# Optimization experiments

Hardware: AMD Instinct MI355X
Metric: run time of the kernel (lower is better)

Reference implementation:

```python
import jax, jax.numpy as jnp
import numpy as np


def setup_inputs() -> dict:
    key = jax.random.key(0)
    k1, k2, k3 = jax.random.split(key, 3)
    B, C, N, T = 32, 64, 1024, 64
    x = jax.random.normal(k1, (B, C, N, T), dtype=jnp.float32)
    W = jax.random.normal(k2, (T, T), dtype=jnp.float32) * 0.05
    alpha = jax.random.normal(k3, (C,), dtype=jnp.float32) * 0.1
    return {"x": x, "W": W, "alpha": alpha}


def reference(x, W, alpha):
    # x: [B, C, N, T]; channel-weighted reduction -> Q = K: [B, N, T]
    q = jnp.einsum('bcnt,c->bnt', x, alpha)
    # bilinear scores: K @ W @ Q^T -> [B, N, N]
    scores = jnp.einsum('bnt,ts,bms->bnm', q, W, q)
    return jax.nn.softmax(scores, axis=-1)
```

## Files before the change

kernel.cpp:

```cpp
#include <hip/hip_runtime.h>

#define B_ 32
#define C_ 64
#define N_ 1024
#define T_ 64

typedef __attribute__((ext_vector_type(8))) _Float16 half8;
typedef __attribute__((ext_vector_type(4))) _Float16 half4;
typedef __attribute__((ext_vector_type(4))) float f32x4;

__global__ __launch_bounds__(256) void k_q(const float* __restrict__ x,
                                           const float* __restrict__ alpha,
                                           _Float16* __restrict__ q_h) {
    const int bid = blockIdx.x;
    const int s1  = (bid & 7) * 256 + (bid >> 3);
    const int b   = s1 >> 6;
    const int n0  = (s1 & 63) * 16;
    const int tid = threadIdx.x;

    const f32x4* xb = (const f32x4*)(x + (size_t)b * C_ * N_ * T_
                                       + (size_t)n0 * T_);
    f32x4 acc = {0.f, 0.f, 0.f, 0.f};
#pragma unroll 4
    for (int c = 0; c < C_; ++c) {
        f32x4 v = __builtin_nontemporal_load(&xb[(size_t)c * (N_ * T_ / 4) + tid]);
        const float ac = alpha[c];
        acc[0] += ac * v[0]; acc[1] += ac * v[1];
        acc[2] += ac * v[2]; acc[3] += ac * v[3];
    }

    half4 h;
#pragma unroll
    for (int j = 0; j < 4; ++j) h[j] = (_Float16)acc[j];
    *(half4*)(q_h + ((size_t)b * N_ + n0) * T_ + (size_t)tid * 4) = h;
}

__global__ __launch_bounds__(512, 4) void k_scores_softmax(
        const _Float16* __restrict__ q_h,
        const float* __restrict__ W,
        float* __restrict__ out) {
    const int bid = blockIdx.x;
    const int s   = (bid & 7) * 128 + (bid >> 3);
    const int b   = s >> 5;
    const int n0  = (s & 31) * 32;
    const int tid  = threadIdx.x;
    const int w    = tid >> 6;
    const int lane = tid & 63;
    const int lr   = lane & 15;
    const int lk   = lane >> 4;

    __shared__ float Ws[T_][T_];
    __shared__ _Float16 qwh[32][72];
    __shared__ float red[32][8];

    {
        const f32x4* Wv = (const f32x4*)W;
        f32x4* Wd = (f32x4*)&Ws[0][0];
        Wd[tid]       = Wv[tid];
        Wd[tid + 512] = Wv[tid + 512];
    }
    __syncthreads();

    {
        const int tr = w >> 2, tc = w & 3;
        const size_t ar = ((size_t)b * N_ + n0 + tr * 16 + lr) * T_ + lk * 8;
        half8 a0 = *(const half8*)(q_h + ar);
        half8 a1 = *(const half8*)(q_h + ar + 32);
        half8 bh0, bh1, bl0, bl1;
#pragma unroll
        for (int j = 0; j < 8; ++j) {
            const float wv0 = Ws[lk * 8 + j][tc * 16 + lr];
            const float wv1 = Ws[lk * 8 + 32 + j][tc * 16 + lr];
            const _Float16 h0 = (_Float16)wv0;
            const _Float16 h1 = (_Float16)wv1;
            bh0[j] = h0; bl0[j] = (_Float16)(wv0 - (float)h0);
            bh1[j] = h1; bl1[j] = (_Float16)(wv1 - (float)h1);
        }
        f32x4 a = {0.f, 0.f, 0.f, 0.f};
        a = __builtin_amdgcn_mfma_f32_16x16x32_f16(a0, bh0, a, 0, 0, 0);
        a = __builtin_amdgcn_mfma_f32_16x16x32_f16(a1, bh1, a, 0, 0, 0);
        a = __builtin_amdgcn_mfma_f32_16x16x32_f16(a0, bl0, a, 0, 0, 0);
        a = __builtin_amdgcn_mfma_f32_16x16x32_f16(a1, bl1, a, 0, 0, 0);
#pragma unroll
        for (int r = 0; r < 4; ++r)
            qwh[tr * 16 + lk * 4 + r][tc * 16 + lr] = (_Float16)a[r];
    }
    __syncthreads();

    half8 af[2][2];
#pragma unroll
    for (int g = 0; g < 2; ++g) {
        af[g][0] = *(const half8*)&qwh[g * 16 + lr][lk * 8];
        af[g][1] = *(const half8*)&qwh[g * 16 + lr][lk * 8 + 32];
    }

    const size_t cb0 = ((size_t)b * N_ + w * 128 + lr) * T_ + lk * 8;

#pragma unroll
    for (int g = 0; g < 2; ++g) {
        f32x4 acc[8];
#pragma unroll
        for (int cf = 0; cf < 8; ++cf) acc[cf] = {0.f, 0.f, 0.f, 0.f};

        half8 pb0 = *(const half8*)(q_h + cb0);
        half8 pb1 = *(const half8*)(q_h + cb0 + 32);
#pragma unroll
        for (int cf = 0; cf < 8; ++cf) {
            const half8 bh0 = pb0;
            const half8 bh1 = pb1;
            if (cf < 7) {
                const size_t cbn = cb0 + (size_t)(cf + 1) * 16 * T_;
                pb0 = *(const half8*)(q_h + cbn);
                pb1 = *(const half8*)(q_h + cbn + 32);
            }
            f32x4 a = acc[cf];
            a = __builtin_amdgcn_mfma_f32_16x16x32_f16(bh0, af[g][0], a, 0, 0, 0);
            a = __builtin_amdgcn_mfma_f32_16x16x32_f16(bh1, af[g][1], a, 0, 0, 0);
            acc[cf] = a;
        }

        float ssum = 0.f;
#pragma unroll
        for (int cf = 0; cf < 8; ++cf) {
#pragma unroll
            for (int r = 0; r < 4; ++r) {
                float e = __expf(acc[cf][r]);
                acc[cf][r] = e;
                ssum += e;
            }
        }
        ssum += __shfl_xor(ssum, 16);
        ssum += __shfl_xor(ssum, 32);
        if (lane < 16) red[g * 16 + lr][w] = ssum;
        __syncthreads();

        f32x4 p0 = *(f32x4*)&red[g * 16 + lr][0];
        f32x4 p1 = *(f32x4*)&red[g * 16 + lr][4];
        const float inv = 1.0f / (p0[0] + p0[1] + p0[2] + p0[3] +
                                  p1[0] + p1[1] + p1[2] + p1[3]);
        f32x4* orow = (f32x4*)(out + ((size_t)b * N_ + n0 + g * 16 + lr) * N_
                                   + w * 128 + lk * 4);
#pragma unroll
        for (int cf = 0; cf < 8; ++cf) {
            f32x4 v = acc[cf];
            v[0] *= inv; v[1] *= inv; v[2] *= inv; v[3] *= inv;
            orow[cf * 4] = v;
        }
    }
}

extern "C" void kernel_launch(void* const* d_in, const int* in_sizes, int n_in,
                              void* d_out, int out_size, void* d_ws, size_t ws_size,
                              hipStream_t stream) {
    const float* x     = (const float*)d_in[0];
    const float* W     = (const float*)d_in[1];
    const float* alpha = (const float*)d_in[2];
    float* out = (float*)d_out;

    _Float16* q_h = (_Float16*)d_ws;

    k_q<<<2048, 256, 0, stream>>>(x, alpha, q_h);
    k_scores_softmax<<<1024, 512, 0, stream>>>(q_h, W, out);
}
```

Before: 134.8 us.

## Double rows per block and keep key fragments in registers across row groups

Each scores block now processes 64 query rows instead of 32, halving the grid. Key fragments are loaded once into registers and reused for all four row groups instead of being reloaded per group. The softmax row-sum buffer is double-buffered, with a lighter LDS barrier between groups. The aim is fewer redundant global reads of q and less per-block setup (W load and conversion), at the cost of higher register pressure and fewer blocks.

Result: faster. 116.9 us (-13.3%).

```diff
diff --git a/kernel.cpp b/kernel.cpp
--- a/kernel.cpp
+++ b/kernel.cpp
@@ -40,9 +40,9 @@
         const float* __restrict__ W,
         float* __restrict__ out) {
     const int bid = blockIdx.x;
-    const int s   = (bid & 7) * 128 + (bid >> 3);
-    const int b   = s >> 5;
-    const int n0  = (s & 31) * 32;
+    const int s   = (bid & 7) * 64 + (bid >> 3);
+    const int b   = s >> 4;
+    const int n0  = (s & 15) * 64;
     const int tid  = threadIdx.x;
     const int w    = tid >> 6;
     const int lane = tid & 63;
@@ -50,8 +50,8 @@
     const int lk   = lane >> 4;
 
     __shared__ float Ws[T_][T_];
-    __shared__ _Float16 qwh[32][72];
-    __shared__ float red[32][8];
+    __shared__ _Float16 qwh[64][72];
+    __shared__ float red[2][16][8];
 
     {
         const f32x4* Wv = (const f32x4*)W;
@@ -62,10 +62,8 @@
     __syncthreads();
 
     {
-        const int tr = w >> 2, tc = w & 3;
-        const size_t ar = ((size_t)b * N_ + n0 + tr * 16 + lr) * T_ + lk * 8;
-        half8 a0 = *(const half8*)(q_h + ar);
-        half8 a1 = *(const half8*)(q_h + ar + 32);
+        const int tc  = w & 3;
+        const int tr0 = (w >> 2) * 2;
         half8 bh0, bh1, bl0, bl1;
 #pragma unroll
         for (int j = 0; j < 8; ++j) {
@@ -76,46 +74,47 @@
             bh0[j] = h0; bl0[j] = (_Float16)(wv0 - (float)h0);
             bh1[j] = h1; bl1[j] = (_Float16)(wv1 - (float)h1);
         }
-        f32x4 a = {0.f, 0.f, 0.f, 0.f};
-        a = __builtin_amdgcn_mfma_f32_16x16x32_f16(a0, bh0, a, 0, 0, 0);
-        a = __builtin_amdgcn_mfma_f32_16x16x32_f16(a1, bh1, a, 0, 0, 0);
-        a = __builtin_amdgcn_mfma_f32_16x16x32_f16(a0, bl0, a, 0, 0, 0);
-        a = __builtin_amdgcn_mfma_f32_16x16x32_f16(a1, bl1, a, 0, 0, 0);
 #pragma unroll
-        for (int r = 0; r < 4; ++r)
-            qwh[tr * 16 + lk * 4 + r][tc * 16 + lr] = (_Float16)a[r];
+        for (int i = 0; i < 2; ++i) {
+            const int tr = tr0 + i;
+            const size_t ar = ((size_t)b * N_ + n0 + tr * 16 + lr) * T_ + lk * 8;
+            half8 a0 = *(const half8*)(q_h + ar);
+            half8 a1 = *(const half8*)(q_h + ar + 32);
+            f32x4 a = {0.f, 0.f, 0.f, 0.f};
+            a = __builtin_amdgcn_mfma_f32_16x16x32_f16(a0, bh0, a, 0, 0, 0);
+            a = __builtin_amdgcn_mfma_f32_16x16x32_f16(a1, bh1, a, 0, 0, 0);
+            a = __builtin_amdgcn_mfma_f32_16x16x32_f16(a0, bl0, a, 0, 0, 0);
+            a = __builtin_amdgcn_mfma_f32_16x16x32_f16(a1, bl1, a, 0, 0, 0);
+#pragma unroll
+            for (int r = 0; r < 4; ++r)
+                qwh[tr * 16 + lk * 4 + r][tc * 16 + lr] = (_Float16)a[r];
+        }
+    }
+
+    half8 bst0[8], bst1[8];
+    {
+        const size_t cb0 = ((size_t)b * N_ + w * 128 + lr) * T_ + lk * 8;
+#pragma unroll
+        for (int cf = 0; cf < 8; ++cf) {
+            bst0[cf] = *(const half8*)(q_h + cb0 + (size_t)cf * 16 * T_);
+            bst1[cf] = *(const half8*)(q_h + cb0 + (size_t)cf * 16 * T_ + 32);
+        }
     }
     __syncthreads();
 
-    half8 af[2][2];
-#pragma unroll
-    for (int g = 0; g < 2; ++g) {
-        af[g][0] = *(const half8*)&qwh[g * 16 + lr][lk * 8];
-        af[g][1] = *(const half8*)&qwh[g * 16 + lr][lk * 8 + 32];
-    }
+    float* const obase = out + ((size_t)b * N_ + n0 + lr) * N_ + w * 128 + lk * 4;
 
-    const size_t cb0 = ((size_t)b * N_ + w * 128 + lr) * T_ + lk * 8;
+#pragma unroll 1
+    for (int g = 0; g < 4; ++g) {
+        half8 af0 = *(const half8*)&qwh[g * 16 + lr][lk * 8];
+        half8 af1 = *(const half8*)&qwh[g * 16 + lr][lk * 8 + 32];
 
-#pragma unroll
-    for (int g = 0; g < 2; ++g) {
         f32x4 acc[8];
 #pragma unroll
-        for (int cf = 0; cf < 8; ++cf) acc[cf] = {0.f, 0.f, 0.f, 0.f};
-
-        half8 pb0 = *(const half8*)(q_h + cb0);
-        half8 pb1 = *(const half8*)(q_h + cb0 + 32);
-#pragma unroll
         for (int cf = 0; cf < 8; ++cf) {
-            const half8 bh0 = pb0;
-            const half8 bh1 = pb1;
-            if (cf < 7) {
-                const size_t cbn = cb0 + (size_t)(cf + 1) * 16 * T_;
-                pb0 = *(const half8*)(q_h + cbn);
-                pb1 = *(const half8*)(q_h + cbn + 32);
-            }
-            f32x4 a = acc[cf];
-            a = __builtin_amdgcn_mfma_f32_16x16x32_f16(bh0, af[g][0], a, 0, 0, 0);
-            a = __builtin_amdgcn_mfma_f32_16x16x32_f16(bh1, af[g][1], a, 0, 0, 0);
+            f32x4 a = {0.f, 0.f, 0.f, 0.f};
+            a = __builtin_amdgcn_mfma_f32_16x16x32_f16(bst0[cf], af0, a, 0, 0, 0);
+            a = __builtin_amdgcn_mfma_f32_16x16x32_f16(bst1[cf], af1, a, 0, 0, 0);
             acc[cf] = a;
         }
 
@@ -131,15 +130,17 @@
         }
         ssum += __shfl_xor(ssum, 16);
         ssum += __shfl_xor(ssum, 32);
-        if (lane < 16) red[g * 16 + lr][w] = ssum;
-        __syncthreads();
+        if (lane < 16) red[g & 1][lr][w] = ssum;
 
-        f32x4 p0 = *(f32x4*)&red[g * 16 + lr][0];
-        f32x4 p1 = *(f32x4*)&red[g * 16 + lr][4];
+        asm volatile("s_waitcnt lgkmcnt(0)" ::: "memory");
+        __builtin_amdgcn_s_barrier();
+        asm volatile("" ::: "memory");
+
+        f32x4 p0 = *(f32x4*)&red[g & 1][lr][0];
+        f32x4 p1 = *(f32x4*)&red[g & 1][lr][4];
         const float inv = 1.0f / (p0[0] + p0[1] + p0[2] + p0[3] +
                                   p1[0] + p1[1] + p1[2] + p1[3]);
-        f32x4* orow = (f32x4*)(out + ((size_t)b * N_ + n0 + g * 16 + lr) * N_
-                                   + w * 128 + lk * 4);
+        f32x4* orow = (f32x4*)(obase + (size_t)g * 16 * N_);
 #pragma unroll
         for (int cf = 0; cf < 8; ++cf) {
             f32x4 v = acc[cf];
@@ -160,5 +161,5 @@
     _Float16* q_h = (_Float16*)d_ws;
 
     k_q<<<2048, 256, 0, stream>>>(x, alpha, q_h);
-    k_scores_softmax<<<1024, 512, 0, stream>>>(q_h, W, out);
+    k_scores_softmax<<<512, 512, 0, stream>>>(q_h, W, out);
 }
```
